# Kernel optimization log

Hardware: AMD Instinct MI355X
Metric: run time of the kernel (lower is better)

Reference implementation:

```python
import jax, jax.numpy as jnp
import numpy as np

LOG2 = float(np.log(2.0))

def ssp(x):
    # shifted softplus: softplus(x) - log(2)
    return jax.nn.softplus(x) - LOG2

def setup_inputs() -> dict:
    key = jax.random.key(0)
    ks = jax.random.split(key, 12)
    B, N, K, G, Fdim, H, O = 2, 1024, 64, 64, 128, 4, 128
    s = 0.05
    return {
        'x': jax.random.normal(ks[0], (B, N, Fdim), jnp.float32),
        'r_ij': jax.random.uniform(ks[1], (B, N, K), jnp.float32),
        'neighbors': jax.random.randint(ks[2], (B, N, K), 0, N),
        'pairwise_mask': jnp.ones((B, N, K), jnp.float32),
        'f_ij': jax.random.normal(ks[3], (B, N, K, G), jnp.float32),
        'w_in2f': jax.random.normal(ks[4], (H, Fdim, Fdim), jnp.float32) * s,
        'w_att': jax.random.normal(ks[5], (H, 2 * Fdim), jnp.float32) * s,
        'wf1': jax.random.normal(ks[6], (G, Fdim), jnp.float32) * s,
        'bf1': jnp.zeros((Fdim,), jnp.float32),
        'wf2': jax.random.normal(ks[7], (Fdim, Fdim), jnp.float32) * s,
        'bf2': jnp.zeros((Fdim,), jnp.float32),
        'w_out': jax.random.normal(ks[8], (Fdim, O), jnp.float32) * s,
        'b_out': jnp.zeros((O,), jnp.float32),
    }

def reference(x, r_ij, neighbors, pairwise_mask, f_ij,
              w_in2f, w_att, wf1, bf1, wf2, bf2, w_out, b_out):
    B, N, K = neighbors.shape
    H, _, Fdim = w_in2f.shape
    # continuous filter network: MLP on radial features -> [B,N,K,F]
    W = ssp(jnp.einsum('bnkg,gf->bnkf', f_ij, wf1) + bf1)
    W = jnp.einsum('bnkf,fe->bnke', W, wf2) + bf2
    # per-head linear projections: [B,H,N,F]
    y = jnp.einsum('bni,hif->bhnf', x, w_in2f)
    # gather neighbor features along atom axis: [B,H,N,K,F]
    idx = jnp.broadcast_to(neighbors.reshape(B, 1, N * K, 1), (B, H, N * K, Fdim))
    y_nb = jnp.take_along_axis(y, idx, axis=2).reshape(B, H, N, K, Fdim)
    # GAT attention logits via split weight (equiv. to concat + Dense):
    a_c = jnp.einsum('bhnf,hf->bhn', y, w_att[:, :Fdim])       # center part
    a_n = jnp.einsum('bhnkf,hf->bhnk', y_nb, w_att[:, Fdim:])  # neighbor part
    att = a_c[:, :, :, None] + a_n                             # [B,H,N,K]
    alpha = jax.nn.softmax(ssp(att), axis=-1)
    # attention-weighted neighbor features times continuous filters, mean over heads
    out = jnp.einsum('bhnk,bhnkf,bnkf->bnkf', alpha, y_nb, W) / H
    # masked aggregation over the neighbor axis
    agg = jnp.sum(out * pairwise_mask[..., None], axis=2)      # [B,N,F]
    return ssp(jnp.einsum('bnf,fo->bno', agg, w_out) + b_out)
```

## Files before the change

### kernel.cpp

```cpp
#include <hip/hip_runtime.h>

#define NB 2
#define NN 1024
#define NK 64
#define NG 64
#define NF 128
#define NH 4
#define NO 128
#define PITCH 132

typedef unsigned short ushort_t;
typedef __attribute__((ext_vector_type(8))) short short8v;
typedef __attribute__((ext_vector_type(4))) float f32x4;

union FragU { uint4 u4; short8v s8; };

__device__ __forceinline__ float bf2f(ushort_t u) {
    union { unsigned int i; float f; } v; v.i = ((unsigned int)u) << 16; return v.f;
}
__device__ __forceinline__ ushort_t f2bf(float f) {
    unsigned int u = __float_as_uint(f);
    unsigned int r = 0x7fffu + ((u >> 16) & 1u);
    return (ushort_t)((u + r) >> 16);
}
__device__ __forceinline__ float sspf(float x) {
    const float u = __builtin_amdgcn_exp2f(-fabsf(x) * 1.44269504088896341f);
    return fmaxf(x, 0.f) + fmaf(0.69314718055994531f,
                                __builtin_amdgcn_logf(1.f + u),
                                -0.69314718055994531f);
}

__global__ __launch_bounds__(256) void k_prep(
    const float* __restrict__ wf1, const float* __restrict__ wf2,
    const float* __restrict__ w_out,
    ushort_t* __restrict__ wf1f, ushort_t* __restrict__ wf2f,
    float* __restrict__ w_outT)
{
    int s = blockIdx.x * 256 + threadIdx.x;
    if (s >= 7168) return;
    if (s >= 3072) {
        const int s2 = s - 3072;
        const int o = s2 >> 5, fb = s2 & 31;
        #pragma unroll
        for (int j = 0; j < 4; ++j)
            w_outT[(size_t)o * NF + fb * 4 + j] = w_out[(size_t)(fb * 4 + j) * NO + o];
        return;
    }
    const float* W; ushort_t* out; int loOff;
    if (s < 1024) { W = wf1; out = wf1f; loOff = 8192; }
    else          { s -= 1024; W = wf2; out = wf2f; loOff = 16384; }
    const int fi = s >> 6, lane = s & 63;
    const int ks = fi >> 3, nf = fi & 7;
    const int n = nf * 16 + (lane & 15);
    const int kb = ks * 32 + ((lane >> 4) & 3) * 4;
    #pragma unroll
    for (int j = 0; j < 8; ++j) {
        const int k = kb + (j & 3) + ((j >> 2) << 4);
        const float v = W[(size_t)k * NF + n];
        const ushort_t hb = f2bf(v);
        out[(size_t)(fi * 64 + lane) * 8 + j] = hb;
        out[(size_t)loOff + (fi * 64 + lane) * 8 + j] = f2bf(v - bf2f(hb));
    }
}

__global__ __launch_bounds__(256) void k_proj(
    const float* __restrict__ x,
    const float* __restrict__ w_in2f,
    const float* __restrict__ w_att,
    ushort_t* __restrict__ y,
    float* __restrict__ a_c,
    float* __restrict__ a_n)
{
    const int bn0 = blockIdx.x * 8;
    const int t = threadIdx.x;
    __shared__ float xs[8][NF];
    __shared__ float ys[32][PITCH];

    {
        const float4* src = (const float4*)(x + (size_t)bn0 * NF);
        float4* dst = (float4*)(&xs[0][0]);
        dst[t] = src[t];
    }
    __syncthreads();

    const int hp = t >> 7;
    const int f0 = t & 127;
    const int h0 = hp, h1 = hp + 2;
    const float* w0 = w_in2f + (size_t)h0 * NF * NF + f0;
    const float* w1 = w_in2f + (size_t)h1 * NF * NF + f0;
    float acc0[8], acc1[8];
    #pragma unroll
    for (int n = 0; n < 8; ++n) { acc0[n] = 0.f; acc1[n] = 0.f; }

    for (int i0 = 0; i0 < NF; i0 += 4) {
        float4 xv[8];
        #pragma unroll
        for (int n = 0; n < 8; ++n) xv[n] = *(const float4*)&xs[n][i0];
        #pragma unroll
        for (int ii = 0; ii < 4; ++ii) {
            const float wa = w0[(size_t)(i0 + ii) * NF];
            const float wb = w1[(size_t)(i0 + ii) * NF];
            #pragma unroll
            for (int n = 0; n < 8; ++n) {
                const float xi = (&xv[n].x)[ii];
                acc0[n] = fmaf(xi, wa, acc0[n]);
                acc1[n] = fmaf(xi, wb, acc1[n]);
            }
        }
    }
    #pragma unroll
    for (int n = 0; n < 8; ++n) {
        const int bn = bn0 + n;
        const int b = bn >> 10, nn = bn & (NN - 1);
        y[((size_t)(b * NH + h0) * NN + nn) * NF + f0] = f2bf(acc0[n]);
        y[((size_t)(b * NH + h1) * NN + nn) * NF + f0] = f2bf(acc1[n]);
        ys[n * 4 + h0][f0] = acc0[n];
        ys[n * 4 + h1][f0] = acc1[n];
    }
    __syncthreads();

    {
        const int hn = t >> 3, q = t & 7;
        const int h = hn & 3, n = hn >> 2;
        float pc = 0.f, pn = 0.f;
        #pragma unroll
        for (int j = 0; j < 16; ++j) {
            const int f = q + 8 * j;
            const float yv = ys[n * 4 + h][f];
            pc = fmaf(yv, w_att[h * 2 * NF + f], pc);
            pn = fmaf(yv, w_att[h * 2 * NF + NF + f], pn);
        }
        #pragma unroll
        for (int off = 1; off < 8; off <<= 1) {
            pc += __shfl_xor(pc, off, 8);
            pn += __shfl_xor(pn, off, 8);
        }
        if (q == 0) {
            const int bn = bn0 + n;
            const int b = bn >> 10, nn = bn & (NN - 1);
            a_c[(size_t)(b * NH + h) * NN + nn] = pc;
            a_n[(size_t)(b * NH + h) * NN + nn] = pn;
        }
    }
}

__global__ __launch_bounds__(256, 4) void k_main(
    const int*      __restrict__ neighbors,
    const float*    __restrict__ pmask,
    const float*    __restrict__ f_ij,
    const float*    __restrict__ bf1,
    const float*    __restrict__ bf2v,
    const float*    __restrict__ w_outT,
    const float*    __restrict__ b_out,
    const ushort_t* __restrict__ y,
    const float*    __restrict__ a_c,
    const float*    __restrict__ a_n,
    const ushort_t* __restrict__ wf1f,
    const ushort_t* __restrict__ wf2f,
    float*          __restrict__ outp)
{
    const int bn = blockIdx.x;
    const int b = bn >> 10, n_ = bn & (NN - 1);
    const int t = threadIdx.x;

    __shared__ __align__(16) char smem[39680];
    ushort_t* W1   = (ushort_t*)(smem);
    ushort_t* fijh = (ushort_t*)(smem + 16896);
    ushort_t* fijl = (ushort_t*)(smem + 25600);
    float*    W2f  = (float*)(smem);
    float*    aggp = (float*)(smem + 33792);
    float*    aggc = (float*)(smem + 37888);
    float*    alpha = (float*)(smem + 38400);
    int*      nbs   = (int*)(smem + 39424);

    const int wave = t >> 6, lane = t & 63;
    const int lrow = lane & 15;
    const int lq   = (lane >> 4) & 3;
    const int wb   = wave * 32;

    {
        const float4* src = (const float4*)(f_ij + (size_t)bn * NK * NG);
        #pragma unroll
        for (int i = 0; i < 4; ++i) {
            const int e4 = i * 256 + t;
            const float4 v = src[e4];
            const int e = e4 * 4;
            const int row = e >> 6, col = e & 63;
            const ushort_t h0 = f2bf(v.x), h1 = f2bf(v.y), h2 = f2bf(v.z), h3 = f2bf(v.w);
            uint2 ph, pl;
            ph.x = (unsigned)h0 | ((unsigned)h1 << 16);
            ph.y = (unsigned)h2 | ((unsigned)h3 << 16);
            pl.x = (unsigned)f2bf(v.x - bf2f(h0)) | ((unsigned)f2bf(v.y - bf2f(h1)) << 16);
            pl.y = (unsigned)f2bf(v.z - bf2f(h2)) | ((unsigned)f2bf(v.w - bf2f(h3)) << 16);
            *(uint2*)&fijh[row * 68 + col] = ph;
            *(uint2*)&fijl[row * 68 + col] = pl;
        }
    }
    if (t < NK) nbs[t] = neighbors[(size_t)bn * NK + t];
    __syncthreads();

    {
        FragU b1h[2][2], b1l[2][2];
        #pragma unroll
        for (int ks = 0; ks < 2; ++ks)
            #pragma unroll
            for (int nf2 = 0; nf2 < 2; ++nf2) {
                const int fi = ks * 8 + wave * 2 + nf2;
                b1h[ks][nf2].u4 = *((const uint4*)wf1f + fi * 64 + lane);
                b1l[ks][nf2].u4 = *((const uint4*)(wf1f + 8192) + fi * 64 + lane);
            }
        f32x4 acc[4][2];
        #pragma unroll
        for (int mf = 0; mf < 4; ++mf)
            #pragma unroll
            for (int nf2 = 0; nf2 < 2; ++nf2) acc[mf][nf2] = (f32x4)0.f;

        #pragma unroll
        for (int mf = 0; mf < 4; ++mf) {
            const int row = mf * 16 + lrow;
            #pragma unroll
            for (int ks = 0; ks < 2; ++ks) {
                const int cb = ks * 32 + lq * 4;
                FragU ah, al;
                {
                    const uint2 p0 = *(const uint2*)&fijh[row * 68 + cb];
                    const uint2 p1 = *(const uint2*)&fijh[row * 68 + cb + 16];
                    uint4 q; q.x = p0.x; q.y = p0.y; q.z = p1.x; q.w = p1.y; ah.u4 = q;
                }
                {
                    const uint2 p0 = *(const uint2*)&fijl[row * 68 + cb];
                    const uint2 p1 = *(const uint2*)&fijl[row * 68 + cb + 16];
                    uint4 q; q.x = p0.x; q.y = p0.y; q.z = p1.x; q.w = p1.y; al.u4 = q;
                }
                #pragma unroll
                for (int nf2 = 0; nf2 < 2; ++nf2) {
                    acc[mf][nf2] = __builtin_amdgcn_mfma_f32_16x16x32_bf16(ah.s8, b1h[ks][nf2].s8, acc[mf][nf2], 0, 0, 0);
                    acc[mf][nf2] = __builtin_amdgcn_mfma_f32_16x16x32_bf16(ah.s8, b1l[ks][nf2].s8, acc[mf][nf2], 0, 0, 0);
                    acc[mf][nf2] = __builtin_amdgcn_mfma_f32_16x16x32_bf16(al.s8, b1h[ks][nf2].s8, acc[mf][nf2], 0, 0, 0);
                }
            }
        }
        const float bia[2] = { bf1[wb + lrow], bf1[wb + 16 + lrow] };
        #pragma unroll
        for (int mf = 0; mf < 4; ++mf)
            #pragma unroll
            for (int nf2 = 0; nf2 < 2; ++nf2) {
                const int col = wb + nf2 * 16 + lrow;
                #pragma unroll
                for (int r = 0; r < 4; ++r) {
                    const int row = mf * 16 + lq * 4 + r;
                    W1[row * 132 + col] = f2bf(sspf(acc[mf][nf2][r] + bia[nf2]));
                }
            }
    }
    __syncthreads();

    {
        f32x4 acc[4][2];
        #pragma unroll
        for (int mf = 0; mf < 4; ++mf)
            #pragma unroll
            for (int nf2 = 0; nf2 < 2; ++nf2) acc[mf][nf2] = (f32x4)0.f;

        for (int ks = 0; ks < 4; ++ks) {
            FragU b2h[2], b2l[2];
            #pragma unroll
            for (int nf2 = 0; nf2 < 2; ++nf2) {
                const int fi = ks * 8 + wave * 2 + nf2;
                b2h[nf2].u4 = *((const uint4*)wf2f + fi * 64 + lane);
                b2l[nf2].u4 = *((const uint4*)(wf2f + 16384) + fi * 64 + lane);
            }
            const int cb = ks * 32 + lq * 4;
            #pragma unroll
            for (int mf = 0; mf < 4; ++mf) {
                const int row = mf * 16 + lrow;
                FragU ah;
                {
                    const uint2 p0 = *(const uint2*)&W1[row * 132 + cb];
                    const uint2 p1 = *(const uint2*)&W1[row * 132 + cb + 16];
                    uint4 q; q.x = p0.x; q.y = p0.y; q.z = p1.x; q.w = p1.y; ah.u4 = q;
                }
                #pragma unroll
                for (int nf2 = 0; nf2 < 2; ++nf2) {
                    acc[mf][nf2] = __builtin_amdgcn_mfma_f32_16x16x32_bf16(ah.s8, b2h[nf2].s8, acc[mf][nf2], 0, 0, 0);
                    acc[mf][nf2] = __builtin_amdgcn_mfma_f32_16x16x32_bf16(ah.s8, b2l[nf2].s8, acc[mf][nf2], 0, 0, 0);
                }
            }
        }
        __syncthreads();
        const float bia[2] = { bf2v[wb + lrow], bf2v[wb + 16 + lrow] };
        #pragma unroll
        for (int mf = 0; mf < 4; ++mf)
            #pragma unroll
            for (int nf2 = 0; nf2 < 2; ++nf2) {
                const int col = wb + nf2 * 16 + lrow;
                #pragma unroll
                for (int r = 0; r < 4; ++r) {
                    const int row = mf * 16 + lq * 4 + r;
                    W2f[row * 132 + col] = acc[mf][nf2][r] + bia[nf2];
                }
            }
    }

    {
        const int h = wave, k = lane;
        const int nb = nbs[k];
        const float av = a_c[(size_t)(b * NH + h) * NN + n_]
                       + a_n[(size_t)(b * NH + h) * NN + nb];
        const float att = sspf(av);
        float m = att;
        #pragma unroll
        for (int off = 32; off > 0; off >>= 1) m = fmaxf(m, __shfl_xor(m, off, 64));
        const float e = __builtin_amdgcn_exp2f((att - m) * 1.44269504088896341f);
        float s = e;
        #pragma unroll
        for (int off = 32; off > 0; off >>= 1) s += __shfl_xor(s, off, 64);
        alpha[h * 64 + k] = (e / s) * pmask[(size_t)bn * NK + k];
    }
    __syncthreads();

    {
        const int fq = (t & 31) * 4;
        const int kg = t >> 5;
        float4 accv; accv.x = accv.y = accv.z = accv.w = 0.f;
        const ushort_t* yb = y + (size_t)b * NH * NN * NF;
        #pragma unroll 4
        for (int kk = 0; kk < 8; ++kk) {
            const int k = kg * 8 + kk;
            const int nb = nbs[k];
            const ushort_t* yp = yb + (size_t)nb * NF + fq;
            const uint2 u0 = *(const uint2*)(yp);
            const uint2 u1 = *(const uint2*)(yp + (size_t)NN * NF);
            const uint2 u2 = *(const uint2*)(yp + 2 * (size_t)NN * NF);
            const uint2 u3 = *(const uint2*)(yp + 3 * (size_t)NN * NF);
            const float a0 = alpha[0 * 64 + k], a1 = alpha[1 * 64 + k];
            const float a2 = alpha[2 * 64 + k], a3 = alpha[3 * 64 + k];
            float4 s;
            s.x = fmaf(a3, bf2f((ushort_t)(u3.x & 0xffffu)),
                  fmaf(a2, bf2f((ushort_t)(u2.x & 0xffffu)),
                  fmaf(a1, bf2f((ushort_t)(u1.x & 0xffffu)),
                       a0 * bf2f((ushort_t)(u0.x & 0xffffu)))));
            s.y = fmaf(a3, bf2f((ushort_t)(u3.x >> 16)),
                  fmaf(a2, bf2f((ushort_t)(u2.x >> 16)),
                  fmaf(a1, bf2f((ushort_t)(u1.x >> 16)),
                       a0 * bf2f((ushort_t)(u0.x >> 16)))));
            s.z = fmaf(a3, bf2f((ushort_t)(u3.y & 0xffffu)),
                  fmaf(a2, bf2f((ushort_t)(u2.y & 0xffffu)),
                  fmaf(a1, bf2f((ushort_t)(u1.y & 0xffffu)),
                       a0 * bf2f((ushort_t)(u0.y & 0xffffu)))));
            s.w = fmaf(a3, bf2f((ushort_t)(u3.y >> 16)),
                  fmaf(a2, bf2f((ushort_t)(u2.y >> 16)),
                  fmaf(a1, bf2f((ushort_t)(u1.y >> 16)),
                       a0 * bf2f((ushort_t)(u0.y >> 16)))));
            const float4 wv = *(const float4*)&W2f[k * 132 + fq];
            accv.x = fmaf(wv.x, s.x, accv.x);
            accv.y = fmaf(wv.y, s.y, accv.y);
            accv.z = fmaf(wv.z, s.z, accv.z);
            accv.w = fmaf(wv.w, s.w, accv.w);
        }
        *(float4*)&aggp[kg * 128 + fq] = accv;
    }
    __syncthreads();
    if (t < NF) {
        float s = 0.f;
        #pragma unroll
        for (int q = 0; q < 8; ++q) s += aggp[q * 128 + t];
        aggc[t] = s * 0.25f;
    }
    __syncthreads();

    if (t < NO) {
        float z = b_out[t];
        const float4* wr = (const float4*)(w_outT + (size_t)t * NF);
        #pragma unroll 8
        for (int q = 0; q < NF / 4; ++q) {
            const float4 w = wr[q];
            const float4 a = *(const float4*)&aggc[q * 4];
            z = fmaf(a.x, w.x, fmaf(a.y, w.y, fmaf(a.z, w.z, fmaf(a.w, w.w, z))));
        }
        outp[(size_t)bn * NO + t] = sspf(z);
    }
}

extern "C" void kernel_launch(void* const* d_in, const int* in_sizes, int n_in,
                              void* d_out, int out_size, void* d_ws, size_t ws_size,
                              hipStream_t stream) {
    const float* x      = (const float*)d_in[0];
    const int*   nbr    = (const int*)d_in[2];
    const float* pmask  = (const float*)d_in[3];
    const float* f_ij   = (const float*)d_in[4];
    const float* w_in2f = (const float*)d_in[5];
    const float* w_att  = (const float*)d_in[6];
    const float* wf1    = (const float*)d_in[7];
    const float* bf1    = (const float*)d_in[8];
    const float* wf2    = (const float*)d_in[9];
    const float* bf2v   = (const float*)d_in[10];
    const float* w_out  = (const float*)d_in[11];
    const float* b_out  = (const float*)d_in[12];

    ushort_t* yb16  = (ushort_t*)d_ws;
    float*    a_c   = (float*)(yb16 + (size_t)NB * NH * NN * NF);
    float*    a_n   = a_c + (size_t)NB * NH * NN;
    ushort_t* wf1f  = (ushort_t*)(a_n + (size_t)NB * NH * NN);
    ushort_t* wf2f  = wf1f + 16384;
    float*    w_outT = (float*)(wf2f + 32768);

    float* outp = (float*)d_out;

    k_prep<<<28, 256, 0, stream>>>(wf1, wf2, w_out, wf1f, wf2f, w_outT);
    k_proj<<<NB * NN / 8, 256, 0, stream>>>(x, w_in2f, w_att, yb16, a_c, a_n);
    k_main<<<NB * NN, 256, 0, stream>>>(nbr, pmask, f_ij, bf1, bf2v,
                                        w_outT, b_out, yb16, a_c, a_n, wf1f, wf2f, outp);
}
```

Baseline: 64.24 us.

## Load f_ij fragments directly from global, store W2 as bf16, raise occupancy

Drops the shared-memory staging of f_ij and splits each value into hi/lo bf16 fragments in registers straight from global loads, using truncation instead of rounding for the high part. The second filter output W2 is now kept in LDS as bf16 instead of fp32, which roughly halves its footprint. Shared memory per block falls enough that the launch bound goes from 4 to 7 blocks per CU, to improve latency hiding. The cost is lower precision in W2 and uncoalesced, strided global reads of f_ij inside the MFMA loop.

Result: slower. 86.75 us (+35.0%).

```diff
diff --git a/kernel.cpp b/kernel.cpp
--- a/kernel.cpp
+++ b/kernel.cpp
@@ -28,6 +28,25 @@
     return fmaxf(x, 0.f) + fmaf(0.69314718055994531f,
                                 __builtin_amdgcn_logf(1.f + u),
                                 -0.69314718055994531f);
+}
+
+__device__ __forceinline__ void splitFrag(const float4 p0, const float4 p1,
+                                          FragU& ah, FragU& al) {
+    const float vv[8] = {p0.x, p0.y, p0.z, p0.w, p1.x, p1.y, p1.z, p1.w};
+    unsigned hu[8], lu[8];
+    #pragma unroll
+    for (int j = 0; j < 8; ++j) {
+        const unsigned u = __float_as_uint(vv[j]);
+        const unsigned ht = u & 0xffff0000u;
+        hu[j] = ht >> 16;
+        lu[j] = __float_as_uint(vv[j] - __uint_as_float(ht)) >> 16;
+    }
+    uint4 qa, ql;
+    qa.x = hu[0] | (hu[1] << 16); qa.y = hu[2] | (hu[3] << 16);
+    qa.z = hu[4] | (hu[5] << 16); qa.w = hu[6] | (hu[7] << 16);
+    ql.x = lu[0] | (lu[1] << 16); ql.y = lu[2] | (lu[3] << 16);
+    ql.z = lu[4] | (lu[5] << 16); ql.w = lu[6] | (lu[7] << 16);
+    ah.u4 = qa; al.u4 = ql;
 }
 
 __global__ __launch_bounds__(256) void k_prep(
@@ -144,7 +163,7 @@
     }
 }
 
-__global__ __launch_bounds__(256, 4) void k_main(
+__global__ __launch_bounds__(256, 7) void k_main(
     const int*      __restrict__ neighbors,
     const float*    __restrict__ pmask,
     const float*    __restrict__ f_ij,
@@ -163,41 +182,20 @@
     const int b = bn >> 10, n_ = bn & (NN - 1);
     const int t = threadIdx.x;
 
-    __shared__ __align__(16) char smem[39680];
+    __shared__ __align__(16) char smem[22784];
     ushort_t* W1   = (ushort_t*)(smem);
-    ushort_t* fijh = (ushort_t*)(smem + 16896);
-    ushort_t* fijl = (ushort_t*)(smem + 25600);
-    float*    W2f  = (float*)(smem);
-    float*    aggp = (float*)(smem + 33792);
-    float*    aggc = (float*)(smem + 37888);
-    float*    alpha = (float*)(smem + 38400);
-    int*      nbs   = (int*)(smem + 39424);
+    ushort_t* W2   = (ushort_t*)(smem);
+    float*    aggp = (float*)(smem + 16896);
+    float*    aggc = (float*)(smem + 20992);
+    float*    alpha = (float*)(smem + 21504);
+    int*      nbs   = (int*)(smem + 22528);
 
     const int wave = t >> 6, lane = t & 63;
     const int lrow = lane & 15;
     const int lq   = (lane >> 4) & 3;
     const int wb   = wave * 32;
 
-    {
-        const float4* src = (const float4*)(f_ij + (size_t)bn * NK * NG);
-        #pragma unroll
-        for (int i = 0; i < 4; ++i) {
-            const int e4 = i * 256 + t;
-            const float4 v = src[e4];
-            const int e = e4 * 4;
-            const int row = e >> 6, col = e & 63;
-            const ushort_t h0 = f2bf(v.x), h1 = f2bf(v.y), h2 = f2bf(v.z), h3 = f2bf(v.w);
-            uint2 ph, pl;
-            ph.x = (unsigned)h0 | ((unsigned)h1 << 16);
-            ph.y = (unsigned)h2 | ((unsigned)h3 << 16);
-            pl.x = (unsigned)f2bf(v.x - bf2f(h0)) | ((unsigned)f2bf(v.y - bf2f(h1)) << 16);
-            pl.y = (unsigned)f2bf(v.z - bf2f(h2)) | ((unsigned)f2bf(v.w - bf2f(h3)) << 16);
-            *(uint2*)&fijh[row * 68 + col] = ph;
-            *(uint2*)&fijl[row * 68 + col] = pl;
-        }
-    }
     if (t < NK) nbs[t] = neighbors[(size_t)bn * NK + t];
-    __syncthreads();
 
     {
         FragU b1h[2][2], b1l[2][2];
@@ -215,23 +213,17 @@
             #pragma unroll
             for (int nf2 = 0; nf2 < 2; ++nf2) acc[mf][nf2] = (f32x4)0.f;
 
+        const float* fbase = f_ij + (size_t)bn * NK * NG;
         #pragma unroll
         for (int mf = 0; mf < 4; ++mf) {
-            const int row = mf * 16 + lrow;
+            const float* frow = fbase + (mf * 16 + lrow) * NG;
             #pragma unroll
             for (int ks = 0; ks < 2; ++ks) {
                 const int cb = ks * 32 + lq * 4;
+                const float4 p0 = *(const float4*)(frow + cb);
+                const float4 p1 = *(const float4*)(frow + cb + 16);
                 FragU ah, al;
-                {
-                    const uint2 p0 = *(const uint2*)&fijh[row * 68 + cb];
-                    const uint2 p1 = *(const uint2*)&fijh[row * 68 + cb + 16];
-                    uint4 q; q.x = p0.x; q.y = p0.y; q.z = p1.x; q.w = p1.y; ah.u4 = q;
-                }
-                {
-                    const uint2 p0 = *(const uint2*)&fijl[row * 68 + cb];
-                    const uint2 p1 = *(const uint2*)&fijl[row * 68 + cb + 16];
-                    uint4 q; q.x = p0.x; q.y = p0.y; q.z = p1.x; q.w = p1.y; al.u4 = q;
-                }
+                splitFrag(p0, p1, ah, al);
                 #pragma unroll
                 for (int nf2 = 0; nf2 < 2; ++nf2) {
                     acc[mf][nf2] = __builtin_amdgcn_mfma_f32_16x16x32_bf16(ah.s8, b1h[ks][nf2].s8, acc[mf][nf2], 0, 0, 0);
@@ -297,7 +289,7 @@
                 #pragma unroll
                 for (int r = 0; r < 4; ++r) {
                     const int row = mf * 16 + lq * 4 + r;
-                    W2f[row * 132 + col] = acc[mf][nf2][r] + bia[nf2];
+                    W2[row * 132 + col] = f2bf(acc[mf][nf2][r] + bia[nf2]);
                 }
             }
     }
@@ -352,11 +344,11 @@
                   fmaf(a2, bf2f((ushort_t)(u2.y >> 16)),
                   fmaf(a1, bf2f((ushort_t)(u1.y >> 16)),
                        a0 * bf2f((ushort_t)(u0.y >> 16)))));
-            const float4 wv = *(const float4*)&W2f[k * 132 + fq];
-            accv.x = fmaf(wv.x, s.x, accv.x);
-            accv.y = fmaf(wv.y, s.y, accv.y);
-            accv.z = fmaf(wv.z, s.z, accv.z);
-            accv.w = fmaf(wv.w, s.w, accv.w);
+            const uint2 wv = *(const uint2*)&W2[k * 132 + fq];
+            accv.x = fmaf(bf2f((ushort_t)(wv.x & 0xffffu)), s.x, accv.x);
+            accv.y = fmaf(bf2f((ushort_t)(wv.x >> 16)),     s.y, accv.y);
+            accv.z = fmaf(bf2f((ushort_t)(wv.y & 0xffffu)), s.z, accv.z);
+            accv.w = fmaf(bf2f((ushort_t)(wv.y >> 16)),     s.w, accv.w);
         }
         *(float4*)&aggp[kg * 128 + fq] = accv;
     }
```

## Shrink shared memory by aliasing buffers and storing filter output in bf16

Applied to the files above, without the earlier changes.

Cuts shared memory from about 39.7KB to 18.7KB. Buffers are aliased more aggressively: the fij staging, W1, W2 and the aggregation partials now share one region, and extra barriers keep the overlapping phases apart. The second filter-layer output is stored as bf16 instead of fp32. The launch bound is raised to 8 blocks per CU so more blocks can be resident, and the attention logit and mask loads are hoisted early so their latency overlaps the MFMA work. In exchange it adds extra barriers, puts more register pressure on the 8-wave bound, and loses some precision in W2.

Result: slower. 82.16 us (+27.9%).

```diff
diff --git a/kernel.cpp b/kernel.cpp
--- a/kernel.cpp
+++ b/kernel.cpp
@@ -144,7 +144,7 @@
     }
 }
 
-__global__ __launch_bounds__(256, 4) void k_main(
+__global__ __launch_bounds__(256, 8) void k_main(
     const int*      __restrict__ neighbors,
     const float*    __restrict__ pmask,
     const float*    __restrict__ f_ij,
@@ -163,15 +163,15 @@
     const int b = bn >> 10, n_ = bn & (NN - 1);
     const int t = threadIdx.x;
 
-    __shared__ __align__(16) char smem[39680];
+    __shared__ __align__(16) char smem[18688];
+    ushort_t* fijh = (ushort_t*)(smem);
+    ushort_t* fijl = (ushort_t*)(smem + 8704);
     ushort_t* W1   = (ushort_t*)(smem);
-    ushort_t* fijh = (ushort_t*)(smem + 16896);
-    ushort_t* fijl = (ushort_t*)(smem + 25600);
-    float*    W2f  = (float*)(smem);
-    float*    aggp = (float*)(smem + 33792);
-    float*    aggc = (float*)(smem + 37888);
-    float*    alpha = (float*)(smem + 38400);
-    int*      nbs   = (int*)(smem + 39424);
+    ushort_t* W2   = (ushort_t*)(smem);
+    float*    aggp = (float*)(smem);
+    float*    aggc = (float*)(smem + 4096);
+    float*    alpha = (float*)(smem + 17408);
+    int*      nbs   = (int*)(smem + 18432);
 
     const int wave = t >> 6, lane = t & 63;
     const int lrow = lane & 15;
@@ -199,6 +199,11 @@
     if (t < NK) nbs[t] = neighbors[(size_t)bn * NK + t];
     __syncthreads();
 
+    const float avc = a_c[(size_t)(b * NH + wave) * NN + n_];
+    const float avn = a_n[(size_t)(b * NH + wave) * NN + nbs[lane]];
+    const float pmk = pmask[(size_t)bn * NK + lane];
+
+    f32x4 acc[4][2];
     {
         FragU b1h[2][2], b1l[2][2];
         #pragma unroll
@@ -209,7 +214,6 @@
                 b1h[ks][nf2].u4 = *((const uint4*)wf1f + fi * 64 + lane);
                 b1l[ks][nf2].u4 = *((const uint4*)(wf1f + 8192) + fi * 64 + lane);
             }
-        f32x4 acc[4][2];
         #pragma unroll
         for (int mf = 0; mf < 4; ++mf)
             #pragma unroll
@@ -240,6 +244,9 @@
                 }
             }
         }
+    }
+    __syncthreads();
+    {
         const float bia[2] = { bf1[wb + lrow], bf1[wb + 16 + lrow] };
         #pragma unroll
         for (int mf = 0; mf < 4; ++mf)
@@ -256,7 +263,6 @@
     __syncthreads();
 
     {
-        f32x4 acc[4][2];
         #pragma unroll
         for (int mf = 0; mf < 4; ++mf)
             #pragma unroll
@@ -287,7 +293,9 @@
                 }
             }
         }
-        __syncthreads();
+    }
+    __syncthreads();
+    {
         const float bia[2] = { bf2v[wb + lrow], bf2v[wb + 16 + lrow] };
         #pragma unroll
         for (int mf = 0; mf < 4; ++mf)
@@ -297,17 +305,13 @@
                 #pragma unroll
                 for (int r = 0; r < 4; ++r) {
                     const int row = mf * 16 + lq * 4 + r;
-                    W2f[row * 132 + col] = acc[mf][nf2][r] + bia[nf2];
-                }
-            }
-    }
-
-    {
-        const int h = wave, k = lane;
-        const int nb = nbs[k];
-        const float av = a_c[(size_t)(b * NH + h) * NN + n_]
-                       + a_n[(size_t)(b * NH + h) * NN + nb];
-        const float att = sspf(av);
+                    W2[row * 132 + col] = f2bf(acc[mf][nf2][r] + bia[nf2]);
+                }
+            }
+    }
+
+    {
+        const float att = sspf(avc + avn);
         float m = att;
         #pragma unroll
         for (int off = 32; off > 0; off >>= 1) m = fmaxf(m, __shfl_xor(m, off, 64));
@@ -315,14 +319,15 @@
         float s = e;
         #pragma unroll
         for (int off = 32; off > 0; off >>= 1) s += __shfl_xor(s, off, 64);
-        alpha[h * 64 + k] = (e / s) * pmask[(size_t)bn * NK + k];
-    }
-    __syncthreads();
-
+        alpha[wave * 64 + lane] = (e / s) * pmk;
+    }
+    __syncthreads();
+
+    float4 accv;
     {
         const int fq = (t & 31) * 4;
         const int kg = t >> 5;
-        float4 accv; accv.x = accv.y = accv.z = accv.w = 0.f;
+        accv.x = accv.y = accv.z = accv.w = 0.f;
         const ushort_t* yb = y + (size_t)b * NH * NN * NF;
         #pragma unroll 4
         for (int kk = 0; kk < 8; ++kk) {
@@ -352,12 +357,17 @@
                   fmaf(a2, bf2f((ushort_t)(u2.y >> 16)),
                   fmaf(a1, bf2f((ushort_t)(u1.y >> 16)),
                        a0 * bf2f((ushort_t)(u0.y >> 16)))));
-            const float4 wv = *(const float4*)&W2f[k * 132 + fq];
-            accv.x = fmaf(wv.x, s.x, accv.x);
-            accv.y = fmaf(wv.y, s.y, accv.y);
-            accv.z = fmaf(wv.z, s.z, accv.z);
-            accv.w = fmaf(wv.w, s.w, accv.w);
-        }
+            const uint2 wv = *(const uint2*)&W2[k * 132 + fq];
+            accv.x = fmaf(bf2f((ushort_t)(wv.x & 0xffffu)), s.x, accv.x);
+            accv.y = fmaf(bf2f((ushort_t)(wv.x >> 16)),     s.y, accv.y);
+            accv.z = fmaf(bf2f((ushort_t)(wv.y & 0xffffu)), s.z, accv.z);
+            accv.w = fmaf(bf2f((ushort_t)(wv.y >> 16)),     s.w, accv.w);
+        }
+    }
+    __syncthreads();
+    {
+        const int fq = (t & 31) * 4;
+        const int kg = t >> 5;
         *(float4*)&aggp[kg * 128 + fq] = accv;
     }
     __syncthreads();
```
